# Kernel optimization log

Hardware: AMD Instinct MI355X
Metric: run time of the kernel (lower is better)

Reference implementation:

```python
import jax, jax.numpy as jnp
from jax import lax
import numpy as np

HEADS = 8
DIM_HEAD = 64


def setup_inputs() -> dict:
    key = jax.random.key(0)
    ks = jax.random.split(key, 6)
    dim, inner = 256, HEADS * DIM_HEAD
    fmap = jax.random.normal(ks[0], (8, dim, 128, 128), dtype=jnp.float32)
    w_q = jax.random.normal(ks[1], (inner, dim), dtype=jnp.float32) * (dim ** -0.5)
    w_dw = jax.random.normal(ks[2], (dim, 1, 3, 3), dtype=jnp.float32) * (9 ** -0.5)
    w_pw = jax.random.normal(ks[3], (2 * inner, dim), dtype=jnp.float32) * (dim ** -0.5)
    w_out = jax.random.normal(ks[4], (dim, inner), dtype=jnp.float32) * (inner ** -0.5)
    b_out = jnp.zeros((dim,), dtype=jnp.float32)
    return {"fmap": fmap, "w_q": w_q, "w_dw": w_dw, "w_pw": w_pw, "w_out": w_out, "b_out": b_out}


def _linear_attention(fmap, w_q, w_dw, w_pw, w_out, b_out):
    B, C, H, W = fmap.shape
    h, d = HEADS, DIM_HEAD
    scale = d ** -0.5
    N = H * W
    # to_q: 1x1 conv, no bias
    q = jnp.einsum('bcxy,oc->boxy', fmap, w_q)  # [B, h*d, H, W]
    # to_kv: depthwise 3x3 (pad 1) then pointwise 1x1, no bias
    dw = lax.conv_general_dilated(
        fmap, w_dw, window_strides=(1, 1), padding=((1, 1), (1, 1)),
        dimension_numbers=('NCHW', 'OIHW', 'NCHW'), feature_group_count=C)
    kv = jnp.einsum('bcxy,oc->boxy', dw, w_pw)  # [B, 2*h*d, H, W]
    k, v = jnp.split(kv, 2, axis=1)

    def to_bhnc(t):  # b (h c) x y -> (b h) (x y) c
        return t.reshape(B, h, d, N).transpose(0, 1, 3, 2).reshape(B * h, N, d)

    q, k, v = to_bhnc(q), to_bhnc(k), to_bhnc(v)
    q = jax.nn.softmax(q, axis=-1) * scale  # softmax over feature dim
    k = jax.nn.softmax(k, axis=-2)          # softmax over spatial dim
    context = jnp.einsum('bnd,bne->bde', k, v)   # [(B*h), d, d]
    out = jnp.einsum('bnd,bde->bne', q, context)  # [(B*h), N, d]
    # (b h) (x y) d -> b (h d) x y
    out = out.reshape(B, h, N, d).transpose(0, 1, 3, 2).reshape(B, h * d, H, W)
    out = jax.nn.gelu(out, approximate=False)
    out = jnp.einsum('bcxy,oc->boxy', out, w_out) + b_out[None, :, None, None]
    return out


def reference(fmap, w_q, w_dw, w_pw, w_out, b_out):
    return _linear_attention(fmap, w_q, w_dw, w_pw, w_out, b_out)
```

## Files before the change

### kernel.cpp

```cpp
#include <hip/hip_runtime.h>
#include <math.h>

#define NPIX 16384

typedef __bf16 bf16x8 __attribute__((ext_vector_type(8)));
typedef float f32x4 __attribute__((ext_vector_type(4)));
typedef unsigned short u16;
typedef unsigned int u32;

__device__ __forceinline__ u16 f2bf(float f) {
    u32 u = __float_as_uint(f);
    u32 r = (u + 0x7FFFu + ((u >> 16) & 1u)) >> 16;
    return (u16)r;
}
__device__ __forceinline__ float bf2f(u32 s) { return __uint_as_float(s << 16); }
__device__ __forceinline__ u32 pk2(float a, float b) {
    return (u32)f2bf(a) | ((u32)f2bf(b) << 16);
}

__global__ __launch_bounds__(256) void k_cvtw(
    const float* __restrict__ wq, const float* __restrict__ wpw,
    const float* __restrict__ wout,
    u16* __restrict__ wq_b, u16* __restrict__ wpw_b, u16* __restrict__ wout_b)
{
    int id = (blockIdx.x * 256 + threadIdx.x) * 4;
    const float* s; u16* d; int off;
    if (id < 131072)      { s = wq;   d = wq_b;   off = id; }
    else if (id < 393216) { s = wpw;  d = wpw_b;  off = id - 131072; }
    else                  { s = wout; d = wout_b; off = id - 393216; }
    f32x4 v = *(const f32x4*)(s + off);
    uint2 u; u.x = pk2(v[0], v[1]); u.y = pk2(v[2], v[3]);
    *(uint2*)(d + off) = u;
}

__global__ __launch_bounds__(256) void k_conv(
    const float* __restrict__ fmap, const float* __restrict__ wdw,
    u16* __restrict__ fmapT, u16* __restrict__ dwT)
{
    const int t = threadIdx.x;
    const int lane = t & 63, w = t >> 6;
    const int x = blockIdx.x, b = blockIdx.y;

    __shared__ u16 dst[2][128][66];

    const float mLf = (lane == 0) ? 0.f : 1.f;
    const float mRf = (lane == 63) ? 0.f : 1.f;
    const float mTf = (x > 0) ? 1.f : 0.f;
    const float mBf = (x < 127) ? 1.f : 0.f;
    const int dT = (x > 0) ? -128 : 0;
    const int dB = (x < 127) ? 128 : 0;

    const size_t nbase = (size_t)b * NPIX + (size_t)x * 128;

    for (int chunk = 0; chunk < 4; ++chunk) {
        for (int g = 0; g < 4; ++g) {
            const int cl0 = w * 16 + g * 4;
            const int c0 = chunk * 64 + cl0;
            float2 T[4], M[4], B[4];
            #pragma unroll
            for (int i = 0; i < 4; ++i) {
                const float* p = fmap + ((size_t)(b * 256 + c0 + i)) * NPIX + (size_t)x * 128;
                M[i] = ((const float2*)p)[lane];
                T[i] = ((const float2*)(p + dT))[lane];
                B[i] = ((const float2*)(p + dB))[lane];
            }
            #pragma unroll
            for (int i = 0; i < 4; ++i) {
                const float* wc = wdw + (c0 + i) * 9;
                float w0 = wc[0] * mTf, w1 = wc[1] * mTf, w2 = wc[2] * mTf;
                float w3 = wc[3],       w4 = wc[4],       w5 = wc[5];
                float w6 = wc[6] * mBf, w7 = wc[7] * mBf, w8 = wc[8] * mBf;
                float tL = __shfl_up(T[i].y, 1) * mLf;
                float mL_ = __shfl_up(M[i].y, 1) * mLf;
                float bL = __shfl_up(B[i].y, 1) * mLf;
                float tR = __shfl_down(T[i].x, 1) * mRf;
                float mR_ = __shfl_down(M[i].x, 1) * mRf;
                float bR = __shfl_down(B[i].x, 1) * mRf;
                float o0 = w0 * tL     + w1 * T[i].x + w2 * T[i].y
                         + w3 * mL_    + w4 * M[i].x + w5 * M[i].y
                         + w6 * bL     + w7 * B[i].x + w8 * B[i].y;
                float o1 = w0 * T[i].x + w1 * T[i].y + w2 * tR
                         + w3 * M[i].x + w4 * M[i].y + w5 * mR_
                         + w6 * B[i].x + w7 * B[i].y + w8 * bR;
                int cl = cl0 + i;
                dst[0][2 * lane][cl]     = f2bf(M[i].x);
                dst[0][2 * lane + 1][cl] = f2bf(M[i].y);
                dst[1][2 * lane][cl]     = f2bf(o0);
                dst[1][2 * lane + 1][cl] = f2bf(o1);
            }
        }
        __syncthreads();
        #pragma unroll
        for (int T2 = 0; T2 < 2; ++T2) {
            u16* gp = T2 ? dwT : fmapT;
            #pragma unroll
            for (int it = 0; it < 4; ++it) {
                int u = it * 256 + t;
                int y = u >> 3, c8 = (u & 7) * 8;
                const u16* s = &dst[T2][y][c8];
                uint4 val;
                val.x = *(const u32*)(s);
                val.y = *(const u32*)(s + 2);
                val.z = *(const u32*)(s + 4);
                val.w = *(const u32*)(s + 6);
                *(uint4*)(gp + (nbase + y) * 256 + chunk * 64 + c8) = val;
            }
        }
        __syncthreads();
    }
}

__global__ __launch_bounds__(256) void k_proj_kv(
    const u16* __restrict__ dwT, const u16* __restrict__ wpw,
    u16* __restrict__ E, u16* __restrict__ V)
{
    const int t = threadIdx.x;
    const int lane = t & 63, w = t >> 6;
    const int l15 = lane & 15, quad = lane >> 4;
    const int n0 = blockIdx.x * 128;
    const int o0 = blockIdx.y * 128;
    const int b  = blockIdx.z;
    __shared__ __align__(16) u16 sm[2 * 128 * 72];
    u16* As = sm;
    u16* Bs = sm + 128 * 72;
    f32x4 acc[4][4] = {};
    const int mh = (w >> 1) * 64, nh = (w & 1) * 64;
    const u16* wrow = wpw + (size_t)o0 * 256;
    const u16* xrow = dwT + ((size_t)b * NPIX + n0) * 256;
    for (int kc = 0; kc < 4; ++kc) {
        __syncthreads();
        const int g = t & 7;
        #pragma unroll
        for (int p = 0; p < 4; ++p) {
            int row = (t >> 3) + 32 * p;
            *(uint4*)(As + row * 72 + g * 8) = *(const uint4*)(wrow + (size_t)row * 256 + kc * 64 + g * 8);
            *(uint4*)(Bs + row * 72 + g * 8) = *(const uint4*)(xrow + (size_t)row * 256 + kc * 64 + g * 8);
        }
        __syncthreads();
        #pragma unroll
        for (int kk = 0; kk < 64; kk += 32) {
            bf16x8 av[4], bv[4];
            #pragma unroll
            for (int mf = 0; mf < 4; ++mf)
                av[mf] = *(const bf16x8*)(As + (mh + mf * 16 + l15) * 72 + kk + quad * 8);
            #pragma unroll
            for (int nf = 0; nf < 4; ++nf)
                bv[nf] = *(const bf16x8*)(Bs + (nh + nf * 16 + l15) * 72 + kk + quad * 8);
            #pragma unroll
            for (int mf = 0; mf < 4; ++mf)
                #pragma unroll
                for (int nf = 0; nf < 4; ++nf)
                    acc[mf][nf] = __builtin_amdgcn_mfma_f32_16x16x32_bf16(av[mf], bv[nf], acc[mf][nf], 0, 0, 0);
        }
    }
    __syncthreads();
    const bool isE = (o0 < 512);
    u16* ep = sm;
    #pragma unroll
    for (int mf = 0; mf < 4; ++mf)
        #pragma unroll
        for (int nf = 0; nf < 4; ++nf)
            #pragma unroll
            for (int r = 0; r < 4; ++r) {
                int row = mh + mf * 16 + quad * 4 + r;
                int col = nh + nf * 16 + l15;
                float vv = acc[mf][nf][r];
                if (isE) vv = expf(vv);
                ep[row * 136 + col] = f2bf(vv);
            }
    __syncthreads();
    u16* outp = isE ? E : V;
    const int cb = isE ? o0 : (o0 - 512);
    for (int p = 0; p < 4; ++p) {
        int row = (t >> 3) + 32 * p;
        size_t base = ((size_t)b * 512 + cb + row) * NPIX + n0;
        int g2 = (t & 7) * 16;
        *(uint4*)(outp + base + g2)     = *(const uint4*)(ep + row * 136 + g2);
        *(uint4*)(outp + base + g2 + 8) = *(const uint4*)(ep + row * 136 + g2 + 8);
    }
}

__global__ __launch_bounds__(256) void k_context(
    const u16* __restrict__ E, const u16* __restrict__ V,
    float* __restrict__ ctx, float* __restrict__ denom)
{
    const int t = threadIdx.x;
    const int lane = t & 63, w = t >> 6;
    const int l15 = lane & 15, quad = lane >> 4;
    const int nb = blockIdx.x * 512;
    const int bh = blockIdx.y;
    __shared__ __align__(16) u16 sm[2 * 64 * 136];
    u16* As = sm;
    u16* Bs = sm + 64 * 136;
    __shared__ float dsum[64];
    if (t < 64) dsum[t] = 0.f;
    f32x4 acc[4] = {};
    const u16* Vb = V + (size_t)bh * 64 * NPIX;
    const u16* Eb = E + (size_t)bh * 64 * NPIX;
    for (int cch = 0; cch < 4; ++cch) {
        int ns = nb + cch * 128;
        __syncthreads();
        int g = t & 15;
        #pragma unroll
        for (int p = 0; p < 4; ++p) {
            int row = (t >> 4) + 16 * p;
            *(uint4*)(As + row * 136 + g * 8) = *(const uint4*)(Vb + (size_t)row * NPIX + ns + g * 8);
            *(uint4*)(Bs + row * 136 + g * 8) = *(const uint4*)(Eb + (size_t)row * NPIX + ns + g * 8);
        }
        __syncthreads();
        #pragma unroll
        for (int kk = 0; kk < 128; kk += 32) {
            bf16x8 av = *(const bf16x8*)(As + (w * 16 + l15) * 136 + kk + quad * 8);
            #pragma unroll
            for (int nf = 0; nf < 4; ++nf) {
                bf16x8 bv = *(const bf16x8*)(Bs + (nf * 16 + l15) * 136 + kk + quad * 8);
                acc[nf] = __builtin_amdgcn_mfma_f32_16x16x32_bf16(av, bv, acc[nf], 0, 0, 0);
            }
        }
    }
    #pragma unroll
    for (int nf = 0; nf < 4; ++nf)
        #pragma unroll
        for (int r = 0; r < 4; ++r) {
            int e = w * 16 + quad * 4 + r;
            int d = nf * 16 + l15;
            atomicAdd(ctx + ((size_t)bh * 64 + e) * 64 + d, acc[nf][r]);
        }
    for (int d = 0; d < 64; ++d) {
        u32 u = *(const u32*)(Eb + (size_t)d * NPIX + nb + t * 2);
        float s = bf2f(u & 0xFFFFu) + bf2f(u >> 16);
        s += __shfl_xor(s, 1);  s += __shfl_xor(s, 2);  s += __shfl_xor(s, 4);
        s += __shfl_xor(s, 8);  s += __shfl_xor(s, 16); s += __shfl_xor(s, 32);
        if (lane == 0) atomicAdd(dsum + d, s);
    }
    __syncthreads();
    if (t < 64) atomicAdd(denom + bh * 64 + t, dsum[t]);
}

__global__ __launch_bounds__(256) void k_proj_q(
    const u16* __restrict__ fmapT, const u16* __restrict__ wq,
    u16* __restrict__ q)
{
    const int t = threadIdx.x;
    const int lane = t & 63, w = t >> 6;
    const int l15 = lane & 15, quad = lane >> 4;
    const int n0 = blockIdx.x * 128;
    const int o0 = blockIdx.y * 128;
    const int b  = blockIdx.z;
    __shared__ __align__(16) unsigned char smraw[71680];
    u16* As = (u16*)smraw;
    u16* Bs = As + 128 * 72;
    f32x4 acc[4][4] = {};
    const int mh = (w >> 1) * 64, nh = (w & 1) * 64;
    const u16* wrow = wq + (size_t)o0 * 256;
    const u16* xrow = fmapT + ((size_t)b * NPIX + n0) * 256;
    for (int kc = 0; kc < 4; ++kc) {
        __syncthreads();
        const int g = t & 7;
        #pragma unroll
        for (int p = 0; p < 4; ++p) {
            int row = (t >> 3) + 32 * p;
            *(uint4*)(As + row * 72 + g * 8) = *(const uint4*)(wrow + (size_t)row * 256 + kc * 64 + g * 8);
            *(uint4*)(Bs + row * 72 + g * 8) = *(const uint4*)(xrow + (size_t)row * 256 + kc * 64 + g * 8);
        }
        __syncthreads();
        #pragma unroll
        for (int kk = 0; kk < 64; kk += 32) {
            bf16x8 av[4], bv[4];
            #pragma unroll
            for (int mf = 0; mf < 4; ++mf)
                av[mf] = *(const bf16x8*)(As + (mh + mf * 16 + l15) * 72 + kk + quad * 8);
            #pragma unroll
            for (int nf = 0; nf < 4; ++nf)
                bv[nf] = *(const bf16x8*)(Bs + (nh + nf * 16 + l15) * 72 + kk + quad * 8);
            #pragma unroll
            for (int mf = 0; mf < 4; ++mf)
                #pragma unroll
                for (int nf = 0; nf < 4; ++nf)
                    acc[mf][nf] = __builtin_amdgcn_mfma_f32_16x16x32_bf16(av[mf], bv[nf], acc[mf][nf], 0, 0, 0);
        }
    }
    __syncthreads();
    float* ep = (float*)smraw;
    #pragma unroll
    for (int mf = 0; mf < 4; ++mf)
        #pragma unroll
        for (int nf = 0; nf < 4; ++nf)
            #pragma unroll
            for (int r = 0; r < 4; ++r) {
                int row = mh + mf * 16 + quad * 4 + r;
                int col = nh + nf * 16 + l15;
                ep[col * 140 + row] = acc[mf][nf][r];
            }
    __syncthreads();
    const int h0 = blockIdx.y * 2;
    for (int p = 0; p < 8; ++p) {
        int unit = p * 32 + (t >> 3);
        int pix = unit >> 1, hh = unit & 1;
        int d8 = (t & 7) * 8;
        f32x4 v0 = *(const f32x4*)(ep + pix * 140 + hh * 64 + d8);
        f32x4 v1 = *(const f32x4*)(ep + pix * 140 + hh * 64 + d8 + 4);
        float e0 = expf(v0[0]), e1 = expf(v0[1]), e2 = expf(v0[2]), e3 = expf(v0[3]);
        float e4 = expf(v1[0]), e5 = expf(v1[1]), e6 = expf(v1[2]), e7 = expf(v1[3]);
        float s = ((e0 + e1) + (e2 + e3)) + ((e4 + e5) + (e6 + e7));
        s += __shfl_xor(s, 1); s += __shfl_xor(s, 2); s += __shfl_xor(s, 4);
        float r = 0.125f / s;
        uint4 u;
        u.x = pk2(e0 * r, e1 * r); u.y = pk2(e2 * r, e3 * r);
        u.z = pk2(e4 * r, e5 * r); u.w = pk2(e6 * r, e7 * r);
        size_t off = (((size_t)b * 8 + h0 + hh) * NPIX + n0 + pix) * 64 + d8;
        *(uint4*)(q + off) = u;
    }
}

__global__ __launch_bounds__(256) void k_attnout(
    const u16* __restrict__ q, const float* __restrict__ ctx,
    const float* __restrict__ denom, const u16* __restrict__ wout,
    const float* __restrict__ bout, float* __restrict__ out)
{
    const int t = threadIdx.x;
    const int lane = t & 63, w = t >> 6;
    const int l15 = lane & 15, quad = lane >> 4;
    const int n0 = blockIdx.x * 32;
    const int b  = blockIdx.y;
    __shared__ __align__(16) u16 tmp[32 * 520];
    __shared__ __align__(16) unsigned char R[20480];
    u16* qs = (u16*)R;
    u16* cs = (u16*)(R + 4608);
    u16* ws = (u16*)R;
    for (int h = 0; h < 8; ++h) {
        __syncthreads();
        {
            int row = t >> 3, g = t & 7;
            *(uint4*)(qs + row * 72 + g * 8) =
                *(const uint4*)(q + (((size_t)b * 8 + h) * NPIX + n0 + row) * 64 + g * 8);
        }
        const int bh = b * 8 + h;
        #pragma unroll
        for (int p = 0; p < 4; ++p) {
            int idx = p * 256 + t;
            int e = idx >> 4, dq = (idx & 15) * 4;
            f32x4 c4 = *(const f32x4*)(ctx + ((size_t)bh * 64 + e) * 64 + dq);
            f32x4 d4 = *(const f32x4*)(denom + bh * 64 + dq);
            uint2 u;
            u.x = pk2(c4[0] / d4[0], c4[1] / d4[1]);
            u.y = pk2(c4[2] / d4[2], c4[3] / d4[3]);
            *(uint2*)(cs + e * 72 + dq) = u;
        }
        __syncthreads();
        f32x4 a1[2] = {};
        #pragma unroll
        for (int kk = 0; kk < 64; kk += 32) {
            bf16x8 av = *(const bf16x8*)(qs + ((w & 1) * 16 + l15) * 72 + kk + quad * 8);
            #pragma unroll
            for (int j = 0; j < 2; ++j) {
                int nf = (w >> 1) * 2 + j;
                bf16x8 bv = *(const bf16x8*)(cs + (nf * 16 + l15) * 72 + kk + quad * 8);
                a1[j] = __builtin_amdgcn_mfma_f32_16x16x32_bf16(av, bv, a1[j], 0, 0, 0);
            }
        }
        #pragma unroll
        for (int j = 0; j < 2; ++j)
            #pragma unroll
            for (int r = 0; r < 4; ++r) {
                int pix = (w & 1) * 16 + quad * 4 + r;
                int e = ((w >> 1) * 2 + j) * 16 + l15;
                float x = a1[j][r];
                float gel = 0.5f * x * (1.0f + erff(x * 0.70710678118654752f));
                tmp[pix * 520 + h * 64 + e] = f2bf(gel);
            }
    }
    __syncthreads();
    f32x4 acc[4][2] = {};
    for (int kc = 0; kc < 16; ++kc) {
        __syncthreads();
        #pragma unroll
        for (int p = 0; p < 4; ++p) {
            int c = (t >> 2) + 64 * p, g = t & 3;
            *(uint4*)(ws + c * 40 + g * 8) = *(const uint4*)(wout + (size_t)c * 512 + kc * 32 + g * 8);
        }
        __syncthreads();
        bf16x8 av[4], bv[2];
        #pragma unroll
        for (int mf = 0; mf < 4; ++mf)
            av[mf] = *(const bf16x8*)(ws + (w * 64 + mf * 16 + l15) * 40 + quad * 8);
        #pragma unroll
        for (int nf = 0; nf < 2; ++nf)
            bv[nf] = *(const bf16x8*)(tmp + (nf * 16 + l15) * 520 + kc * 32 + quad * 8);
        #pragma unroll
        for (int mf = 0; mf < 4; ++mf)
            #pragma unroll
            for (int nf = 0; nf < 2; ++nf)
                acc[mf][nf] = __builtin_amdgcn_mfma_f32_16x16x32_bf16(av[mf], bv[nf], acc[mf][nf], 0, 0, 0);
    }
    #pragma unroll
    for (int mf = 0; mf < 4; ++mf)
        #pragma unroll
        for (int nf = 0; nf < 2; ++nf)
            #pragma unroll
            for (int r = 0; r < 4; ++r) {
                int c = w * 64 + mf * 16 + quad * 4 + r;
                int pix = nf * 16 + l15;
                out[((size_t)b * 256 + c) * NPIX + n0 + pix] = acc[mf][nf][r] + bout[c];
            }
}

extern "C" void kernel_launch(void* const* d_in, const int* in_sizes, int n_in,
                              void* d_out, int out_size, void* d_ws, size_t ws_size,
                              hipStream_t stream)
{
    const float* fmap  = (const float*)d_in[0];
    const float* w_q   = (const float*)d_in[1];
    const float* w_dw  = (const float*)d_in[2];
    const float* w_pw  = (const float*)d_in[3];
    const float* w_out = (const float*)d_in[4];
    const float* b_out = (const float*)d_in[5];
    float* out = (float*)d_out;
    char* ws = (char*)d_ws;

    u16* dwT     = (u16*)(ws);
    u16* fmapT   = (u16*)(ws + 67108864);
    u16* E       = (u16*)(ws + 134217728);
    u16* V       = (u16*)(ws + 268435456);
    u16* q       = (u16*)(ws + 134217728);
    float* ctx   = (float*)(ws + 402653184);
    float* denom = (float*)(ws + 403701760);
    u16* wq_b    = (u16*)(ws + 403718144);
    u16* wpw_b   = (u16*)(ws + 403980288);
    u16* wout_b  = (u16*)(ws + 404504576);

    hipMemsetAsync(ws + 402653184, 0, 1048576 + 16384, stream);
    k_cvtw<<<512, 256, 0, stream>>>(w_q, w_pw, w_out, wq_b, wpw_b, wout_b);
    k_conv<<<dim3(128, 8), 256, 0, stream>>>(fmap, w_dw, fmapT, dwT);
    k_proj_kv<<<dim3(128, 8, 8), 256, 0, stream>>>(dwT, wpw_b, E, V);
    k_context<<<dim3(32, 64), 256, 0, stream>>>(E, V, ctx, denom);
    k_proj_q<<<dim3(128, 4, 8), 256, 0, stream>>>(fmapT, wq_b, q);
    k_attnout<<<dim3(512, 8), 256, 0, stream>>>(q, ctx, denom, wout_b, b_out, out);
}
```

Baseline: 900.5 us.

## Fuse KV projection with context accumulation to skip E/V global round-trip

```diff
diff --git a/kernel.cpp b/kernel.cpp
--- a/kernel.cpp
+++ b/kernel.cpp
@@ -110,111 +110,94 @@
     }
 }
 
-__global__ __launch_bounds__(256) void k_proj_kv(
+__global__ __launch_bounds__(256) void k_kvctx(
     const u16* __restrict__ dwT, const u16* __restrict__ wpw,
-    u16* __restrict__ E, u16* __restrict__ V)
+    float* __restrict__ ctx, float* __restrict__ denom)
 {
     const int t = threadIdx.x;
     const int lane = t & 63, w = t >> 6;
     const int l15 = lane & 15, quad = lane >> 4;
-    const int n0 = blockIdx.x * 128;
-    const int o0 = blockIdx.y * 128;
-    const int b  = blockIdx.z;
-    __shared__ __align__(16) u16 sm[2 * 128 * 72];
-    u16* As = sm;
-    u16* Bs = sm + 128 * 72;
-    f32x4 acc[4][4] = {};
-    const int mh = (w >> 1) * 64, nh = (w & 1) * 64;
-    const u16* wrow = wpw + (size_t)o0 * 256;
-    const u16* xrow = dwT + ((size_t)b * NPIX + n0) * 256;
-    for (int kc = 0; kc < 4; ++kc) {
-        __syncthreads();
-        const int g = t & 7;
-        #pragma unroll
-        for (int p = 0; p < 4; ++p) {
-            int row = (t >> 3) + 32 * p;
-            *(uint4*)(As + row * 72 + g * 8) = *(const uint4*)(wrow + (size_t)row * 256 + kc * 64 + g * 8);
-            *(uint4*)(Bs + row * 72 + g * 8) = *(const uint4*)(xrow + (size_t)row * 256 + kc * 64 + g * 8);
-        }
-        __syncthreads();
-        #pragma unroll
-        for (int kk = 0; kk < 64; kk += 32) {
-            bf16x8 av[4], bv[4];
-            #pragma unroll
-            for (int mf = 0; mf < 4; ++mf)
-                av[mf] = *(const bf16x8*)(As + (mh + mf * 16 + l15) * 72 + kk + quad * 8);
-            #pragma unroll
-            for (int nf = 0; nf < 4; ++nf)
-                bv[nf] = *(const bf16x8*)(Bs + (nh + nf * 16 + l15) * 72 + kk + quad * 8);
-            #pragma unroll
-            for (int mf = 0; mf < 4; ++mf)
+
+    const int L = blockIdx.x;
+    const int work = (L & 7) * 64 + (L >> 3);
+    const int s = work >> 6;
+    const int b = (work >> 3) & 7;
+    const int h = work & 7;
+    const int bh = b * 8 + h;
+
+    __shared__ __align__(16) u16 As[128 * 72];
+    __shared__ __align__(16) u16 Bs[128 * 72];
+    __shared__ __align__(16) u16 EL[64 * 136];
+    __shared__ __align__(16) u16 VL[64 * 136];
+
+    const int ph = (w & 1) * 64;
+    const int ck = (w >> 1);
+
+    f32x4 ctxacc[4] = {};
+    f32x4 dacc[4] = {};
+    union { u16 a[8]; bf16x8 v; } uo;
+    #pragma unroll
+    for (int i = 0; i < 8; ++i) uo.a[i] = 0x3F80;
+    const bf16x8 ones = uo.v;
+
+    for (int st = 0; st < 16; ++st) {
+        const int n0 = s * 2048 + st * 128;
+        const u16* xrow = dwT + ((size_t)b * NPIX + n0) * 256;
+        f32x4 acc[4][4] = {};
+        for (int kc = 0; kc < 4; ++kc) {
+            __syncthreads();
+            const int g = t & 7;
+            #pragma unroll
+            for (int p = 0; p < 4; ++p) {
+                int row = (t >> 3) + 32 * p;
+                int wr = (row < 64) ? (h * 64 + row) : (512 + h * 64 + (row - 64));
+                *(uint4*)(As + row * 72 + g * 8) = *(const uint4*)(wpw + (size_t)wr * 256 + kc * 64 + g * 8);
+                *(uint4*)(Bs + row * 72 + g * 8) = *(const uint4*)(xrow + (size_t)row * 256 + kc * 64 + g * 8);
+            }
+            __syncthreads();
+            #pragma unroll
+            for (int kk = 0; kk < 64; kk += 32) {
+                bf16x8 av[4], bv[4];
+                #pragma unroll
+                for (int mf = 0; mf < 4; ++mf)
+                    av[mf] = *(const bf16x8*)(Bs + (ph + mf * 16 + l15) * 72 + kk + quad * 8);
                 #pragma unroll
                 for (int nf = 0; nf < 4; ++nf)
-                    acc[mf][nf] = __builtin_amdgcn_mfma_f32_16x16x32_bf16(av[mf], bv[nf], acc[mf][nf], 0, 0, 0);
-        }
-    }
-    __syncthreads();
-    const bool isE = (o0 < 512);
-    u16* ep = sm;
-    #pragma unroll
-    for (int mf = 0; mf < 4; ++mf)
-        #pragma unroll
-        for (int nf = 0; nf < 4; ++nf)
-            #pragma unroll
-            for (int r = 0; r < 4; ++r) {
-                int row = mh + mf * 16 + quad * 4 + r;
-                int col = nh + nf * 16 + l15;
-                float vv = acc[mf][nf][r];
-                if (isE) vv = expf(vv);
-                ep[row * 136 + col] = f2bf(vv);
-            }
-    __syncthreads();
-    u16* outp = isE ? E : V;
-    const int cb = isE ? o0 : (o0 - 512);
-    for (int p = 0; p < 4; ++p) {
-        int row = (t >> 3) + 32 * p;
-        size_t base = ((size_t)b * 512 + cb + row) * NPIX + n0;
-        int g2 = (t & 7) * 16;
-        *(uint4*)(outp + base + g2)     = *(const uint4*)(ep + row * 136 + g2);
-        *(uint4*)(outp + base + g2 + 8) = *(const uint4*)(ep + row * 136 + g2 + 8);
-    }
-}
-
-__global__ __launch_bounds__(256) void k_context(
-    const u16* __restrict__ E, const u16* __restrict__ V,
-    float* __restrict__ ctx, float* __restrict__ denom)
-{
-    const int t = threadIdx.x;
-    const int lane = t & 63, w = t >> 6;
-    const int l15 = lane & 15, quad = lane >> 4;
-    const int nb = blockIdx.x * 512;
-    const int bh = blockIdx.y;
-    __shared__ __align__(16) u16 sm[2 * 64 * 136];
-    u16* As = sm;
-    u16* Bs = sm + 64 * 136;
-    __shared__ float dsum[64];
-    if (t < 64) dsum[t] = 0.f;
-    f32x4 acc[4] = {};
-    const u16* Vb = V + (size_t)bh * 64 * NPIX;
-    const u16* Eb = E + (size_t)bh * 64 * NPIX;
-    for (int cch = 0; cch < 4; ++cch) {
-        int ns = nb + cch * 128;
-        __syncthreads();
-        int g = t & 15;
-        #pragma unroll
-        for (int p = 0; p < 4; ++p) {
-            int row = (t >> 4) + 16 * p;
-            *(uint4*)(As + row * 136 + g * 8) = *(const uint4*)(Vb + (size_t)row * NPIX + ns + g * 8);
-            *(uint4*)(Bs + row * 136 + g * 8) = *(const uint4*)(Eb + (size_t)row * NPIX + ns + g * 8);
-        }
-        __syncthreads();
-        #pragma unroll
-        for (int kk = 0; kk < 128; kk += 32) {
-            bf16x8 av = *(const bf16x8*)(As + (w * 16 + l15) * 136 + kk + quad * 8);
+                    bv[nf] = *(const bf16x8*)(As + (ck * 64 + nf * 16 + l15) * 72 + kk + quad * 8);
+                #pragma unroll
+                for (int mf = 0; mf < 4; ++mf)
+                    #pragma unroll
+                    for (int nf = 0; nf < 4; ++nf)
+                        acc[mf][nf] = __builtin_amdgcn_mfma_f32_16x16x32_bf16(av[mf], bv[nf], acc[mf][nf], 0, 0, 0);
+            }
+        }
+        u16* dst = ck ? VL : EL;
+        #pragma unroll
+        for (int nf = 0; nf < 4; ++nf) {
+            const int ch = nf * 16 + l15;
+            #pragma unroll
+            for (int mf = 0; mf < 4; ++mf) {
+                const int px = ph + mf * 16 + quad * 4;
+                float v0 = acc[mf][nf][0], v1 = acc[mf][nf][1];
+                float v2 = acc[mf][nf][2], v3 = acc[mf][nf][3];
+                if (ck == 0) {
+                    v0 = __expf(v0); v1 = __expf(v1);
+                    v2 = __expf(v2); v3 = __expf(v3);
+                }
+                uint2 u; u.x = pk2(v0, v1); u.y = pk2(v2, v3);
+                *(uint2*)(dst + ch * 136 + px) = u;
+            }
+        }
+        __syncthreads();
+        #pragma unroll
+        for (int kk2 = 0; kk2 < 128; kk2 += 32) {
+            bf16x8 av = *(const bf16x8*)(VL + (w * 16 + l15) * 136 + kk2 + quad * 8);
             #pragma unroll
             for (int nf = 0; nf < 4; ++nf) {
-                bf16x8 bv = *(const bf16x8*)(Bs + (nf * 16 + l15) * 136 + kk + quad * 8);
-                acc[nf] = __builtin_amdgcn_mfma_f32_16x16x32_bf16(av, bv, acc[nf], 0, 0, 0);
+                bf16x8 bv = *(const bf16x8*)(EL + (nf * 16 + l15) * 136 + kk2 + quad * 8);
+                ctxacc[nf] = __builtin_amdgcn_mfma_f32_16x16x32_bf16(av, bv, ctxacc[nf], 0, 0, 0);
+                if (w == 0)
+                    dacc[nf] = __builtin_amdgcn_mfma_f32_16x16x32_bf16(ones, bv, dacc[nf], 0, 0, 0);
             }
         }
     }
@@ -224,17 +207,13 @@
         for (int r = 0; r < 4; ++r) {
             int e = w * 16 + quad * 4 + r;
             int d = nf * 16 + l15;
-            atomicAdd(ctx + ((size_t)bh * 64 + e) * 64 + d, acc[nf][r]);
-        }
-    for (int d = 0; d < 64; ++d) {
-        u32 u = *(const u32*)(Eb + (size_t)d * NPIX + nb + t * 2);
-        float s = bf2f(u & 0xFFFFu) + bf2f(u >> 16);
-        s += __shfl_xor(s, 1);  s += __shfl_xor(s, 2);  s += __shfl_xor(s, 4);
-        s += __shfl_xor(s, 8);  s += __shfl_xor(s, 16); s += __shfl_xor(s, 32);
-        if (lane == 0) atomicAdd(dsum + d, s);
-    }
-    __syncthreads();
-    if (t < 64) atomicAdd(denom + bh * 64 + t, dsum[t]);
+            atomicAdd(ctx + ((size_t)bh * 64 + e) * 64 + d, ctxacc[nf][r]);
+        }
+    if (w == 0 && quad == 0) {
+        #pragma unroll
+        for (int nf = 0; nf < 4; ++nf)
+            atomicAdd(denom + bh * 64 + nf * 16 + l15, dacc[nf][0]);
+    }
 }
 
 __global__ __launch_bounds__(256) void k_proj_q(
@@ -300,8 +279,8 @@
         int d8 = (t & 7) * 8;
         f32x4 v0 = *(const f32x4*)(ep + pix * 140 + hh * 64 + d8);
         f32x4 v1 = *(const f32x4*)(ep + pix * 140 + hh * 64 + d8 + 4);
-        float e0 = expf(v0[0]), e1 = expf(v0[1]), e2 = expf(v0[2]), e3 = expf(v0[3]);
-        float e4 = expf(v1[0]), e5 = expf(v1[1]), e6 = expf(v1[2]), e7 = expf(v1[3]);
+        float e0 = __expf(v0[0]), e1 = __expf(v0[1]), e2 = __expf(v0[2]), e3 = __expf(v0[3]);
+        float e4 = __expf(v1[0]), e5 = __expf(v1[1]), e6 = __expf(v1[2]), e7 = __expf(v1[3]);
         float s = ((e0 + e1) + (e2 + e3)) + ((e4 + e5) + (e6 + e7));
         s += __shfl_xor(s, 1); s += __shfl_xor(s, 2); s += __shfl_xor(s, 4);
         float r = 0.125f / s;
@@ -420,8 +399,6 @@
 
     u16* dwT     = (u16*)(ws);
     u16* fmapT   = (u16*)(ws + 67108864);
-    u16* E       = (u16*)(ws + 134217728);
-    u16* V       = (u16*)(ws + 268435456);
     u16* q       = (u16*)(ws + 134217728);
     float* ctx   = (float*)(ws + 402653184);
     float* denom = (float*)(ws + 403701760);
@@ -432,8 +409,7 @@
     hipMemsetAsync(ws + 402653184, 0, 1048576 + 16384, stream);
     k_cvtw<<<512, 256, 0, stream>>>(w_q, w_pw, w_out, wq_b, wpw_b, wout_b);
     k_conv<<<dim3(128, 8), 256, 0, stream>>>(fmap, w_dw, fmapT, dwT);
-    k_proj_kv<<<dim3(128, 8, 8), 256, 0, stream>>>(dwT, wpw_b, E, V);
-    k_context<<<dim3(32, 64), 256, 0, stream>>>(E, V, ctx, denom);
+    k_kvctx<<<512, 256, 0, stream>>>(dwT, wpw_b, ctx, denom);
     k_proj_q<<<dim3(128, 4, 8), 256, 0, stream>>>(fmapT, wq_b, q);
     k_attnout<<<dim3(512, 8), 256, 0, stream>>>(q, ctx, denom, wout_b, b_out, out);
 }
```

New measurement: 806.4 us. 10.4% less time.
